# Performance work log

Hardware: AMD Instinct MI355X
Metric: run time of the kernel (lower is better)

The kernel has to match this reference:

```python
import jax, jax.numpy as jnp
import numpy as np
from math import sqrt

B, N, CS, H, D, K = 8, 256, 512, 8, 64, 32
NB = 2 * K + 1          # no_bins = 65
CT = 2048               # c_transition
INF = 1e9
WL = sqrt(0.5)          # w_L
EPS = 1e-5


def setup_inputs() -> dict:
    key = jax.random.key(0)
    ks = jax.random.split(key, 10)
    sc = 0.02
    return {
        "s": jax.random.normal(ks[0], (B, N, CS), jnp.float32),
        "masks": jnp.ones((B, N), jnp.bool_),
        "wq": jax.random.normal(ks[1], (CS, D * H), jnp.float32) * sc,
        "wk": jax.random.normal(ks[2], (CS, D * H), jnp.float32) * sc,
        "wv": jax.random.normal(ks[3], (CS, D * H), jnp.float32) * sc,
        "wb": jax.random.normal(ks[4], (NB, H), jnp.float32) * sc,
        "wo": jax.random.normal(ks[5], ((NB + D) * H, CS), jnp.float32) * sc,
        "bo": jnp.zeros((CS,), jnp.float32),
        "ln1_g": jnp.ones((CS,), jnp.float32),
        "ln1_b": jnp.zeros((CS,), jnp.float32),
        "w1": jax.random.normal(ks[6], (CS, CT), jnp.float32) * sc,
        "b1": jnp.zeros((CT,), jnp.float32),
        "w2": jax.random.normal(ks[7], (CT, CS), jnp.float32) * sc,
        "b2": jnp.zeros((CS,), jnp.float32),
        "ln2_g": jnp.ones((CS,), jnp.float32),
        "ln2_b": jnp.zeros((CS,), jnp.float32),
    }


def _layernorm(x, g, b):
    m = jnp.mean(x, -1, keepdims=True)
    v = jnp.var(x, -1, keepdims=True)
    return (x - m) * jax.lax.rsqrt(v + EPS) * g + b


def _heads(x):  # [B,N,D*H] -> [B,H,N,D]  (torch: reshape(B,N,D,H) then move H forward)
    return jnp.transpose(x.reshape(B, N, D, H), (0, 3, 1, 2))


def reference(s, masks, wq, wk, wv, wb, wo, bo, ln1_g, ln1_b, w1, b1, w2, b2, ln2_g, ln2_b):
    mf = masks.astype(s.dtype)                       # [B,N]
    sq = mf[:, :, None] * mf[:, None, :]             # [B,N,N]

    # relative position one-hot, clipped to [-K, K] -> [N,N,NB]
    r = jnp.arange(N)
    dmat = jnp.clip(r[:, None] - r[None, :], -K, K) + K
    relpos_base = jax.nn.one_hot(dmat, NB, dtype=s.dtype)
    relpos = relpos_base[None] * sq[..., None]       # [B,N,N,NB]

    b_bias = jnp.einsum('bijc,ch->bhij', relpos, wb)  # [B,H,N,N]

    q = _heads(s @ wq)                               # [B,H,N,D]
    k = _heads(s @ wk)
    v = _heads(s @ wv)

    logits = WL * (jnp.einsum('bhid,bhjd->bhij', q, k) / sqrt(D) + b_bias)
    logits = logits - INF * (1.0 - sq)[:, None]      # mask
    a = jax.nn.softmax(logits, axis=-1)              # [B,H,N,N]

    # pairwise aggregation and value aggregation (einsum avoids [B,H,N,N,NB] blowup)
    o_pair = jnp.einsum('bhij,bijc->bhic', a, relpos)  # [B,H,N,NB]
    o = jnp.einsum('bhij,bhjd->bhid', a, v)            # [B,H,N,D]

    op = jnp.transpose(o_pair, (0, 2, 1, 3)).reshape(B, N, H * NB)
    ov = jnp.transpose(o, (0, 2, 1, 3)).reshape(B, N, H * D)
    embd = jnp.concatenate([op, ov], axis=-1) @ wo + bo   # [B,N,CS]

    x = _layernorm(s + embd, ln1_g, ln1_b)
    ff = jax.nn.relu(x @ w1 + b1) @ w2 + b2
    x = _layernorm(x + ff, ln2_g, ln2_b)
    return x, a
```

## Files before the change

kernel.cpp:

```cpp
#include <hip/hip_runtime.h>
#include <hip/hip_bf16.h>
#include <cstdint>

#define B_ 8
#define N_ 256
#define CS_ 512
#define H_ 8
#define D_ 64
#define K_ 32
#define NB_ 65
#define CT_ 2048
#define WL_ 0.70710678118654752f

typedef __attribute__((ext_vector_type(8))) short bf16x8;
typedef __attribute__((ext_vector_type(4))) float f32x4;

#define GLOBAL_AS __attribute__((address_space(1)))
#define LDS_AS __attribute__((address_space(3)))

__device__ __forceinline__ void async16(void* lds, const void* g) {
  __builtin_amdgcn_global_load_lds((const GLOBAL_AS uint32_t*)g,
                                   (LDS_AS uint32_t*)lds, 16, 0, 0);
}

__device__ __forceinline__ ushort f2bf(float v) {
  __hip_bfloat16 hb = __float2bfloat16(v);
  return *(ushort*)&hb;
}

__device__ __forceinline__ float bf2f(ushort u) {
  union { uint32_t ui; float f; } cv; cv.ui = (uint32_t)u << 16;
  return cv.f;
}

__global__ __launch_bounds__(128) void gemm_bf16(
    const ushort* __restrict__ A, const ushort* __restrict__ Bt,
    const float* __restrict__ bias, float* __restrict__ C,
    ushort* __restrict__ Cb, int M, int Nc, int Kd, int flags) {
  __shared__ ushort As[2][64 * 64];
  __shared__ ushort Bs[2][128 * 64];
  int tid = threadIdx.x;
  int bm = blockIdx.y * 64, bn = blockIdx.x * 128;
  int S = gridDim.z, z = blockIdx.z;
  int T = Kd >> 6;
  int it0 = (z * T) / S, it1 = ((z + 1) * T) / S;
  if (flags & 8)  C  += (size_t)z * M * Nc;
  if (flags & 32) Cb += (size_t)z * M * Nc;
  int w = tid >> 6, l = tid & 63;
  int lm = l & 15, lq = l >> 4;
  int srow = tid >> 3;
  int sg = tid & 7;

  f32x4 acc[4][4];
#pragma unroll
  for (int i = 0; i < 4; ++i)
#pragma unroll
    for (int j = 0; j < 4; ++j) acc[i][j] = (f32x4){0.f, 0.f, 0.f, 0.f};

  {
    int k0 = it0 << 6;
#pragma unroll
    for (int r = 0; r < 4; ++r) {
      int row = r * 16 + srow;
      int gl = sg ^ (row & 7);
      async16(&As[0][row * 64 + sg * 8],
              A + (size_t)(bm + row) * Kd + k0 + gl * 8);
    }
#pragma unroll
    for (int r = 0; r < 8; ++r) {
      int row = r * 16 + srow;
      int gl = sg ^ (row & 7);
      async16(&Bs[0][row * 64 + sg * 8],
              Bt + (size_t)(bn + row) * Kd + k0 + gl * 8);
    }
  }
  for (int it = it0; it < it1; ++it) {
    int cur = (it - it0) & 1;
    __syncthreads();
    if (it + 1 < it1) {
      int nxt = cur ^ 1;
      int k0 = (it + 1) << 6;
#pragma unroll
      for (int r = 0; r < 4; ++r) {
        int row = r * 16 + srow;
        int gl = sg ^ (row & 7);
        async16(&As[nxt][row * 64 + sg * 8],
                A + (size_t)(bm + row) * Kd + k0 + gl * 8);
      }
#pragma unroll
      for (int r = 0; r < 8; ++r) {
        int row = r * 16 + srow;
        int gl = sg ^ (row & 7);
        async16(&Bs[nxt][row * 64 + sg * 8],
                Bt + (size_t)(bn + row) * Kd + k0 + gl * 8);
      }
    }
#pragma unroll
    for (int kk = 0; kk < 2; ++kk) {
      bf16x8 af[4], bfr[4];
#pragma unroll
      for (int i = 0; i < 4; ++i) {
        int ma = 16 * i + lm;
        af[i] = *(const bf16x8*)&As[cur][ma * 64 + ((kk * 4 + lq) ^ (ma & 7)) * 8];
        int nb = w * 64 + 16 * i + lm;
        bfr[i] = *(const bf16x8*)&Bs[cur][nb * 64 + ((kk * 4 + lq) ^ (nb & 7)) * 8];
      }
#pragma unroll
      for (int i = 0; i < 4; ++i)
#pragma unroll
        for (int j = 0; j < 4; ++j)
          acc[i][j] = __builtin_amdgcn_mfma_f32_16x16x32_bf16(
              af[i], bfr[j], acc[i][j], 0, 0, 0);
    }
  }
  __syncthreads();

  int bcol0 = bn + w * 64;
  int lr = l >> 3, lc = l & 7;
  ushort* Tb = &Bs[0][w * 4096];

  if (flags & 16) {
    int which = bcol0 >> 9;
    int hh = (bcol0 & 511) >> 6;
    int b = bm >> 8, nn0 = bm & 255;
    if (which == 2) {
#pragma unroll
      for (int j = 0; j < 4; ++j)
#pragma unroll
        for (int i = 0; i < 4; ++i) {
          ushort pk[4];
#pragma unroll
          for (int r = 0; r < 4; ++r) pk[r] = f2bf(acc[i][j][r]);
          *(uint2*)&Tb[(16 * j + lm) * 64 + 16 * i + lq * 4] = *(uint2*)pk;
        }
    } else {
#pragma unroll
      for (int j = 0; j < 4; ++j)
#pragma unroll
        for (int i = 0; i < 4; ++i)
#pragma unroll
          for (int r = 0; r < 4; ++r)
            Tb[(16 * i + lq * 4 + r) * 64 + 16 * j + lm] = f2bf(acc[i][j][r]);
    }
    __asm__ __volatile__("" ::: "memory");
    ushort* dstb = Cb + (size_t)which * 1048576 + (size_t)(b * 8 + hh) * 16384;
#pragma unroll
    for (int p = 0; p < 8; ++p) {
      int rowL = p * 8 + lr;
      bf16x8 vv = *(const bf16x8*)&Tb[rowL * 64 + lc * 8];
      if (which == 2)
        *(bf16x8*)(dstb + (size_t)rowL * 256 + nn0 + lc * 8) = vv;
      else
        *(bf16x8*)(dstb + (size_t)(nn0 + rowL) * 64 + lc * 8) = vv;
    }
    return;
  }
  if (flags & 4) {
#pragma unroll
    for (int j = 0; j < 4; ++j) {
      float bv = ((flags & 1) && z == 0) ? bias[bcol0 + 16 * j + lm] : 0.f;
#pragma unroll
      for (int i = 0; i < 4; ++i)
#pragma unroll
        for (int r = 0; r < 4; ++r) {
          float v = acc[i][j][r] + bv;
          if (flags & 2) v = fmaxf(v, 0.f);
          Tb[(16 * i + lq * 4 + r) * 64 + 16 * j + lm] = f2bf(v);
        }
    }
    __asm__ __volatile__("" ::: "memory");
#pragma unroll
    for (int p = 0; p < 8; ++p) {
      int rowL = p * 8 + lr;
      bf16x8 vv = *(const bf16x8*)&Tb[rowL * 64 + lc * 8];
      *(bf16x8*)(Cb + (size_t)(bm + rowL) * Nc + bcol0 + lc * 8) = vv;
    }
    return;
  }
#pragma unroll
  for (int j = 0; j < 4; ++j) {
    int col = bcol0 + 16 * j + lm;
    float bv = ((flags & 1) && z == 0) ? bias[col] : 0.f;
#pragma unroll
    for (int i = 0; i < 4; ++i)
#pragma unroll
      for (int r = 0; r < 4; ++r) {
        int row = bm + 16 * i + lq * 4 + r;
        float v = acc[i][j][r] + bv;
        if (flags & 2) v = fmaxf(v, 0.f);
        C[(size_t)row * Nc + col] = v;
      }
  }
}

__global__ __launch_bounds__(256) void prep_all(
    const float* __restrict__ s, __hip_bfloat16* __restrict__ s_bf,
    const float* __restrict__ wq, const float* __restrict__ wk,
    const float* __restrict__ wv, const float* __restrict__ wo,
    const float* __restrict__ w1, const float* __restrict__ w2,
    __hip_bfloat16* __restrict__ wqkvT, __hip_bfloat16* __restrict__ wopT,
    __hip_bfloat16* __restrict__ w1T, __hip_bfloat16* __restrict__ w2T) {
  int blk = blockIdx.x;
  if (blk < 512) {
    int i = blk * 256 + threadIdx.x;
    float4 a = ((const float4*)s)[i * 2];
    float4 c = ((const float4*)s)[i * 2 + 1];
    ushort pk[8] = {f2bf(a.x), f2bf(a.y), f2bf(a.z), f2bf(a.w),
                    f2bf(c.x), f2bf(c.y), f2bf(c.z), f2bf(c.w)};
    *(uint4*)&((ushort*)s_bf)[i * 8] = *(uint4*)pk;
    return;
  }
  blk -= 512;
  __shared__ float tile[32][33];
  const float* src;
  __hip_bfloat16* dst;
  int R, C, Kpad, tX, tIdx, whichBase = -1;
  if (blk < 768) {
    int zz = blk >> 8; tIdx = blk & 255;
    src = zz == 0 ? wq : zz == 1 ? wk : wv;
    dst = wqkvT; whichBase = zz * 512; R = 512; C = 512; Kpad = 512; tX = 16;
  } else if (blk < 1312) {
    tIdx = blk - 768; src = wo; dst = wopT; R = 1032; C = 512; Kpad = 1088; tX = 16;
  } else if (blk < 2336) {
    tIdx = blk - 1312; src = w1; dst = w1T; R = 512; C = 2048; Kpad = 512; tX = 64;
  } else {
    tIdx = blk - 2336; src = w2; dst = w2T; R = 2048; C = 512; Kpad = 2048; tX = 16;
  }
  int c0 = (tIdx % tX) * 32, r0 = (tIdx / tX) * 32;
  int tx = threadIdx.x & 31, ty = threadIdx.x >> 5;
#pragma unroll
  for (int yy = 0; yy < 32; yy += 8) {
    int r = r0 + ty + yy, c = c0 + tx;
    tile[ty + yy][tx] = (r < R && c < C) ? src[(size_t)r * C + c] : 0.f;
  }
  __syncthreads();
#pragma unroll
  for (int yy = 0; yy < 32; yy += 8) {
    int cc = c0 + ty + yy, k = r0 + tx;
    if (cc < C && k < Kpad) {
      int n = (whichBase >= 0) ? (whichBase + (cc & 7) * 64 + (cc >> 3)) : cc;
      dst[(size_t)n * Kpad + k] = __float2bfloat16(tile[tx][ty + yy]);
    }
  }
}

__global__ __launch_bounds__(128) void attn_fused(
    const ushort* __restrict__ qh, const ushort* __restrict__ kh,
    const ushort* __restrict__ vT, const int* __restrict__ masks,
    const float* __restrict__ wb, float* __restrict__ a_out,
    ushort* __restrict__ cat) {
  int strip = blockIdx.x & 7, bh = blockIdx.x >> 3;
  int h = bh & 7, b = bh >> 3;
  __shared__ ushort Ks[256 * 64];
  __shared__ ushort Ps[32 * 64];
  __shared__ float wbs[NB_];
  __shared__ float mfj[256];
  int tid = threadIdx.x;
  int srow = tid >> 3, sg = tid & 7;
#pragma unroll
  for (int rr = 0; rr < 16; ++rr) {
    int row = rr * 16 + srow;
    int gl = sg ^ (row & 7);
    async16(&Ks[row * 64 + sg * 8],
            kh + ((size_t)bh * 256 + row) * 64 + gl * 8);
  }
  int w = tid >> 6, l = tid & 63, lm = l & 15, lq = l >> 4;
  bf16x8 qf[2];
  {
    const ushort* qrow =
        qh + ((size_t)bh * 256 + strip * 32 + w * 16 + lm) * 64 + lq * 8;
    qf[0] = *(const bf16x8*)qrow;
    qf[1] = *(const bf16x8*)(qrow + 32);
  }
  if (tid < NB_) wbs[tid] = wb[tid * H_ + h];
  mfj[tid]       = (masks[b * 256 + tid] != 0) ? 1.f : 0.f;
  mfj[tid + 128] = (masks[b * 256 + tid + 128] != 0) ? 1.f : 0.f;
  __syncthreads();

  f32x4 acc[16];
#pragma unroll
  for (int ct = 0; ct < 16; ++ct) {
    int krow = ct * 16 + lm;
    bf16x8 kf0 = *(const bf16x8*)&Ks[krow * 64 + ((lq) ^ (krow & 7)) * 8];
    bf16x8 kf1 = *(const bf16x8*)&Ks[krow * 64 + ((4 + lq) ^ (krow & 7)) * 8];
    f32x4 zf = (f32x4){0.f, 0.f, 0.f, 0.f};
    zf = __builtin_amdgcn_mfma_f32_16x16x32_bf16(qf[0], kf0, zf, 0, 0, 0);
    acc[ct] = __builtin_amdgcn_mfma_f32_16x16x32_bf16(qf[1], kf1, zf, 0, 0, 0);
  }
  int ibase = strip * 32 + w * 16 + lq * 4;
  float mfi[4];
#pragma unroll
  for (int r = 0; r < 4; ++r) mfi[r] = mfj[ibase + r];
#pragma unroll
  for (int ct = 0; ct < 16; ++ct) {
    int j = ct * 16 + lm;
    float mj = mfj[j];
#pragma unroll
    for (int r = 0; r < 4; ++r) {
      int i = ibase + r;
      int diff = i - j;
      int cb = diff < -K_ ? 0 : (diff > K_ ? 2 * K_ : diff + K_);
      float sq = mfi[r] * mj;
      acc[ct][r] = WL_ * (acc[ct][r] * 0.125f + wbs[cb] * sq) - 1e9f * (1.f - sq);
    }
  }
  float mx[4], sm[4];
#pragma unroll
  for (int r = 0; r < 4; ++r) {
    float m = acc[0][r];
#pragma unroll
    for (int ct = 1; ct < 16; ++ct) m = fmaxf(m, acc[ct][r]);
#pragma unroll
    for (int o = 1; o < 16; o <<= 1) m = fmaxf(m, __shfl_xor(m, o, 64));
    mx[r] = m;
  }
#pragma unroll
  for (int ct = 0; ct < 16; ++ct)
#pragma unroll
    for (int r = 0; r < 4; ++r) acc[ct][r] = __expf(acc[ct][r] - mx[r]);
#pragma unroll
  for (int r = 0; r < 4; ++r) {
    float s = 0.f;
#pragma unroll
    for (int ct = 0; ct < 16; ++ct) s += acc[ct][r];
#pragma unroll
    for (int o = 1; o < 16; o <<= 1) s += __shfl_xor(s, o, 64);
    sm[r] = 1.f / s;
  }
  float p0[4] = {0.f, 0.f, 0.f, 0.f}, p64[4] = {0.f, 0.f, 0.f, 0.f};
#pragma unroll
  for (int ct = 0; ct < 16; ++ct) {
    int j = ct * 16 + lm;
    float mj = mfj[j];
#pragma unroll
    for (int r = 0; r < 4; ++r) {
      int i = ibase + r;
      float aval = acc[ct][r] * sm[r];
      a_out[((size_t)bh * 256 + i) * 256 + j] = aval;
      float val = aval * mfi[r] * mj;
      int diff = i - j;
      if (diff <= -K_)      p0[r] += val;
      else if (diff >= K_)  p64[r] += val;
      else cat[((size_t)(b * 256 + i)) * 1088 + h * 65 + diff + K_] = f2bf(val);
    }
  }
#pragma unroll
  for (int r = 0; r < 4; ++r)
#pragma unroll
    for (int o = 1; o < 16; o <<= 1) {
      p0[r]  += __shfl_xor(p0[r], o, 64);
      p64[r] += __shfl_xor(p64[r], o, 64);
    }
  if (lm == 0) {
#pragma unroll
    for (int r = 0; r < 4; ++r) {
      int i = ibase + r;
      cat[((size_t)(b * 256 + i)) * 1088 + h * 65 + 0]      = f2bf(p0[r]);
      cat[((size_t)(b * 256 + i)) * 1088 + h * 65 + 2 * K_] = f2bf(p64[r]);
    }
  }
#pragma unroll
  for (int r = 0; r < 4; ++r) {
    int i = ibase + r;
#pragma unroll
    for (int t = 0; t < 4; ++t) {
      int c = 1 + lm + 16 * t;
      if (c < 64) {
        int j = i - c + K_;
        if (j < 0 || j > 255)
          cat[((size_t)(b * 256 + i)) * 1088 + h * 65 + c] = 0;
      }
    }
  }
  if (h == 0) {
    for (int idx = tid; idx < 32 * 56; idx += 128) {
      int r = idx / 56, c = 1032 + (idx - r * 56);
      cat[((size_t)(b * 256 + strip * 32 + r)) * 1088 + c] = 0;
    }
  }
  f32x4 acc2[4];
#pragma unroll
  for (int nt = 0; nt < 4; ++nt) acc2[nt] = (f32x4){0.f, 0.f, 0.f, 0.f};
  const ushort* vbase = vT + (size_t)bh * 16384;
#pragma unroll
  for (int qt = 0; qt < 4; ++qt) {
    bf16x8 vf0[4], vf1[4];
#pragma unroll
    for (int nt = 0; nt < 4; ++nt) {
      const ushort* vrow = vbase + (size_t)(nt * 16 + lm) * 256 + qt * 64 + lq * 8;
      vf0[nt] = *(const bf16x8*)vrow;
      vf1[nt] = *(const bf16x8*)(vrow + 32);
    }
#pragma unroll
    for (int ctl = 0; ctl < 4; ++ctl) {
      int ct = qt * 4 + ctl;
#pragma unroll
      for (int r = 0; r < 4; ++r) {
        int rowl = w * 16 + lq * 4 + r;
        int g = ctl * 2 + (lm >> 3);
        Ps[rowl * 64 + ((g ^ (rowl & 7)) << 3) + (lm & 7)] =
            f2bf(acc[ct][r] * sm[r]);
      }
    }
    int prow = w * 16 + lm;
#pragma unroll
    for (int kst = 0; kst < 2; ++kst) {
      bf16x8 af = *(const bf16x8*)&Ps[prow * 64 + (((kst * 4 + lq) ^ (prow & 7)) << 3)];
#pragma unroll
      for (int nt = 0; nt < 4; ++nt)
        acc2[nt] = __builtin_amdgcn_mfma_f32_16x16x32_bf16(
            af, kst ? vf1[nt] : vf0[nt], acc2[nt], 0, 0, 0);
    }
  }
#pragma unroll
  for (int nt = 0; nt < 4; ++nt) {
    int d = nt * 16 + lm;
#pragma unroll
    for (int r = 0; r < 4; ++r) {
      int i = ibase + r;
      cat[((size_t)(b * 256 + i)) * 1088 + 520 + h * 64 + d] = f2bf(acc2[nt][r]);
    }
  }
}

__global__ __launch_bounds__(128) void ln_sum(
    const float* __restrict__ x1, const ushort* __restrict__ xp,
    int S, int stride, const float* __restrict__ g,
    const float* __restrict__ bta, float* __restrict__ out,
    __hip_bfloat16* __restrict__ out_bf) {
  __shared__ float redA[2], redB[2];
  int row = blockIdx.x, tid = threadIdx.x;
  size_t base = (size_t)row * 512;
  float4 v = *(const float4*)(x1 + base + tid * 4);
  for (int s = 0; s < S; ++s) {
    uint2 p = *(const uint2*)(xp + (size_t)s * stride + base + tid * 4);
    v.x += bf2f((ushort)(p.x & 0xffff));
    v.y += bf2f((ushort)(p.x >> 16));
    v.z += bf2f((ushort)(p.y & 0xffff));
    v.w += bf2f((ushort)(p.y >> 16));
  }
  float su = v.x + v.y + v.z + v.w;
  float sq = v.x * v.x + v.y * v.y + v.z * v.z + v.w * v.w;
#pragma unroll
  for (int o = 32; o > 0; o >>= 1) {
    su += __shfl_xor(su, o, 64);
    sq += __shfl_xor(sq, o, 64);
  }
  int w = tid >> 6;
  if ((tid & 63) == 0) { redA[w] = su; redB[w] = sq; }
  __syncthreads();
  su = redA[0] + redA[1]; sq = redB[0] + redB[1];
  float mean = su * (1.f / 512.f);
  float var = sq * (1.f / 512.f) - mean * mean;
  float inv = rsqrtf(var + 1e-5f);
  float4 gv = *(const float4*)(g + tid * 4);
  float4 bv = *(const float4*)(bta + tid * 4);
  float4 o4;
  o4.x = (v.x - mean) * inv * gv.x + bv.x;
  o4.y = (v.y - mean) * inv * gv.y + bv.y;
  o4.z = (v.z - mean) * inv * gv.z + bv.z;
  o4.w = (v.w - mean) * inv * gv.w + bv.w;
  *(float4*)(out + base + tid * 4) = o4;
  if (out_bf) {
    ushort pk[4] = {f2bf(o4.x), f2bf(o4.y), f2bf(o4.z), f2bf(o4.w)};
    *(uint2*)&((ushort*)out_bf)[base + tid * 4] = *(uint2*)pk;
  }
}

extern "C" void kernel_launch(void* const* d_in, const int* in_sizes, int n_in,
                              void* d_out, int out_size, void* d_ws, size_t ws_size,
                              hipStream_t stream) {
  const float* s     = (const float*)d_in[0];
  const int*   masks = (const int*)d_in[1];
  const float* wq = (const float*)d_in[2];
  const float* wk = (const float*)d_in[3];
  const float* wv = (const float*)d_in[4];
  const float* wb = (const float*)d_in[5];
  const float* wo = (const float*)d_in[6];
  const float* bo = (const float*)d_in[7];
  const float* ln1_g = (const float*)d_in[8];
  const float* ln1_b = (const float*)d_in[9];
  const float* w1 = (const float*)d_in[10];
  const float* b1 = (const float*)d_in[11];
  const float* w2 = (const float*)d_in[12];
  const float* b2 = (const float*)d_in[13];
  const float* ln2_g = (const float*)d_in[14];
  const float* ln2_b = (const float*)d_in[15];

  float* out_x = (float*)d_out;
  float* out_a = out_x + 1048576;

  float* ws = (float*)d_ws;
  ushort* embd_part = (ushort*)(ws + 0);
  float* xbuf       = ws + 4194304;
  ushort* ff_part   = (ushort*)(ws + 5242880);
  ushort* qkv_bf    = (ushort*)(ws + 9437184);
  ushort* q_bf = qkv_bf;
  ushort* k_bf = qkv_bf + 1048576;
  ushort* v_bf = qkv_bf + 2097152;
  ushort* cat_bf = (ushort*)(ws + 10223616);
  __hip_bfloat16* h_bf  = (__hip_bfloat16*)(ws + 11337728);
  __hip_bfloat16* s_bf  = (__hip_bfloat16*)(ws + 13434880);
  __hip_bfloat16* x_bf  = (__hip_bfloat16*)(ws + 13959168);
  __hip_bfloat16* wqkvT = (__hip_bfloat16*)(ws + 14483456);
  __hip_bfloat16* wopT  = (__hip_bfloat16*)(ws + 14876672);
  __hip_bfloat16* w1T   = (__hip_bfloat16*)(ws + 15155200);
  __hip_bfloat16* w2T   = (__hip_bfloat16*)(ws + 15679488);

  dim3 blk(256), blkg(128);
  prep_all<<<dim3(3872), blk, 0, stream>>>(s, s_bf, wq, wk, wv, wo, w1, w2,
                                           wqkvT, wopT, w1T, w2T);
  gemm_bf16<<<dim3(12, 32, 1), blkg, 0, stream>>>(
      (const ushort*)s_bf, (const ushort*)wqkvT, nullptr, nullptr,
      qkv_bf, 2048, 1536, 512, 16);
  attn_fused<<<dim3(512), blkg, 0, stream>>>(q_bf, k_bf, v_bf, masks, wb,
                                             out_a, cat_bf);
  gemm_bf16<<<dim3(4, 32, 4), blkg, 0, stream>>>(
      cat_bf, (const ushort*)wopT, bo, nullptr, embd_part,
      2048, 512, 1088, 1 | 4 | 32);
  ln_sum<<<dim3(2048), blkg, 0, stream>>>(s, embd_part, 4, 1048576,
                                          ln1_g, ln1_b, xbuf, x_bf);
  gemm_bf16<<<dim3(16, 32, 1), blkg, 0, stream>>>(
      (const ushort*)x_bf, (const ushort*)w1T, b1, nullptr, (ushort*)h_bf,
      2048, 2048, 512, 1 | 2 | 4);
  gemm_bf16<<<dim3(4, 32, 4), blkg, 0, stream>>>(
      (const ushort*)h_bf, (const ushort*)w2T, b2, nullptr, ff_part,
      2048, 512, 2048, 1 | 4 | 32);
  ln_sum<<<dim3(2048), blkg, 0, stream>>>(xbuf, ff_part, 4, 1048576,
                                          ln2_g, ln2_b, out_x, nullptr);
}
```

Measured before the change: 178.6 us.

## Fuse all stages into one persistent kernel with software grid barriers

```diff
diff --git a/kernel.cpp b/kernel.cpp
--- a/kernel.cpp
+++ b/kernel.cpp
@@ -11,6 +11,7 @@
 #define NB_ 65
 #define CT_ 2048
 #define WL_ 0.70710678118654752f
+#define NBLK 512
 
 typedef __attribute__((ext_vector_type(8))) short bf16x8;
 typedef __attribute__((ext_vector_type(4))) float f32x4;
@@ -33,18 +34,38 @@
   return cv.f;
 }
 
-__global__ __launch_bounds__(128) void gemm_bf16(
+__device__ unsigned g_cnt = 0, g_gen = 0;
+
+__device__ __forceinline__ void gridbar(int tid) {
+  __syncthreads();
+  if (tid == 0) {
+    unsigned g = __hip_atomic_load(&g_gen, __ATOMIC_RELAXED,
+                                   __HIP_MEMORY_SCOPE_AGENT);
+    unsigned v = __hip_atomic_fetch_add(&g_cnt, 1u, __ATOMIC_ACQ_REL,
+                                        __HIP_MEMORY_SCOPE_AGENT);
+    if (v == NBLK - 1u) {
+      __hip_atomic_store(&g_cnt, 0u, __ATOMIC_RELAXED,
+                         __HIP_MEMORY_SCOPE_AGENT);
+      __hip_atomic_store(&g_gen, g + 1u, __ATOMIC_RELEASE,
+                         __HIP_MEMORY_SCOPE_AGENT);
+    } else {
+      while (__hip_atomic_load(&g_gen, __ATOMIC_RELAXED,
+                               __HIP_MEMORY_SCOPE_AGENT) == g)
+        __builtin_amdgcn_s_sleep(8);
+      __builtin_amdgcn_fence(__ATOMIC_ACQUIRE, "agent");
+    }
+  }
+  __syncthreads();
+}
+
+__device__ __forceinline__ void gemm_stage(
     const ushort* __restrict__ A, const ushort* __restrict__ Bt,
-    const float* __restrict__ bias, float* __restrict__ C,
-    ushort* __restrict__ Cb, int M, int Nc, int Kd, int flags) {
-  __shared__ ushort As[2][64 * 64];
-  __shared__ ushort Bs[2][128 * 64];
-  int tid = threadIdx.x;
-  int bm = blockIdx.y * 64, bn = blockIdx.x * 128;
-  int S = gridDim.z, z = blockIdx.z;
+    const float* __restrict__ bias, ushort* __restrict__ Cb,
+    int M, int Nc, int Kd, int flags, int bx, int by, int z, int S,
+    ushort* As, ushort* Bs, int tid) {
+  int bm = by * 64, bn = bx * 128;
   int T = Kd >> 6;
   int it0 = (z * T) / S, it1 = ((z + 1) * T) / S;
-  if (flags & 8)  C  += (size_t)z * M * Nc;
   if (flags & 32) Cb += (size_t)z * M * Nc;
   int w = tid >> 6, l = tid & 63;
   int lm = l & 15, lq = l >> 4;
@@ -63,14 +84,14 @@
     for (int r = 0; r < 4; ++r) {
       int row = r * 16 + srow;
       int gl = sg ^ (row & 7);
-      async16(&As[0][row * 64 + sg * 8],
+      async16(&As[row * 64 + sg * 8],
               A + (size_t)(bm + row) * Kd + k0 + gl * 8);
     }
 #pragma unroll
     for (int r = 0; r < 8; ++r) {
       int row = r * 16 + srow;
       int gl = sg ^ (row & 7);
-      async16(&Bs[0][row * 64 + sg * 8],
+      async16(&Bs[row * 64 + sg * 8],
               Bt + (size_t)(bn + row) * Kd + k0 + gl * 8);
     }
   }
@@ -84,14 +105,14 @@
       for (int r = 0; r < 4; ++r) {
         int row = r * 16 + srow;
         int gl = sg ^ (row & 7);
-        async16(&As[nxt][row * 64 + sg * 8],
+        async16(&As[nxt * 4096 + row * 64 + sg * 8],
                 A + (size_t)(bm + row) * Kd + k0 + gl * 8);
       }
 #pragma unroll
       for (int r = 0; r < 8; ++r) {
         int row = r * 16 + srow;
         int gl = sg ^ (row & 7);
-        async16(&Bs[nxt][row * 64 + sg * 8],
+        async16(&Bs[nxt * 8192 + row * 64 + sg * 8],
                 Bt + (size_t)(bn + row) * Kd + k0 + gl * 8);
       }
     }
@@ -101,9 +122,11 @@
 #pragma unroll
       for (int i = 0; i < 4; ++i) {
         int ma = 16 * i + lm;
-        af[i] = *(const bf16x8*)&As[cur][ma * 64 + ((kk * 4 + lq) ^ (ma & 7)) * 8];
+        af[i] = *(const bf16x8*)&As[cur * 4096 + ma * 64 +
+                                    ((kk * 4 + lq) ^ (ma & 7)) * 8];
         int nb = w * 64 + 16 * i + lm;
-        bfr[i] = *(const bf16x8*)&Bs[cur][nb * 64 + ((kk * 4 + lq) ^ (nb & 7)) * 8];
+        bfr[i] = *(const bf16x8*)&Bs[cur * 8192 + nb * 64 +
+                                     ((kk * 4 + lq) ^ (nb & 7)) * 8];
       }
 #pragma unroll
       for (int i = 0; i < 4; ++i)
@@ -117,7 +140,7 @@
 
   int bcol0 = bn + w * 64;
   int lr = l >> 3, lc = l & 7;
-  ushort* Tb = &Bs[0][w * 4096];
+  ushort* Tb = Bs + w * 4096;
 
   if (flags & 16) {
     int which = bcol0 >> 9;
@@ -155,107 +178,35 @@
     }
     return;
   }
-  if (flags & 4) {
-#pragma unroll
-    for (int j = 0; j < 4; ++j) {
-      float bv = ((flags & 1) && z == 0) ? bias[bcol0 + 16 * j + lm] : 0.f;
-#pragma unroll
-      for (int i = 0; i < 4; ++i)
-#pragma unroll
-        for (int r = 0; r < 4; ++r) {
-          float v = acc[i][j][r] + bv;
-          if (flags & 2) v = fmaxf(v, 0.f);
-          Tb[(16 * i + lq * 4 + r) * 64 + 16 * j + lm] = f2bf(v);
-        }
-    }
-    __asm__ __volatile__("" ::: "memory");
-#pragma unroll
-    for (int p = 0; p < 8; ++p) {
-      int rowL = p * 8 + lr;
-      bf16x8 vv = *(const bf16x8*)&Tb[rowL * 64 + lc * 8];
-      *(bf16x8*)(Cb + (size_t)(bm + rowL) * Nc + bcol0 + lc * 8) = vv;
-    }
-    return;
-  }
 #pragma unroll
   for (int j = 0; j < 4; ++j) {
-    int col = bcol0 + 16 * j + lm;
-    float bv = ((flags & 1) && z == 0) ? bias[col] : 0.f;
+    float bv = ((flags & 1) && z == 0) ? bias[bcol0 + 16 * j + lm] : 0.f;
 #pragma unroll
     for (int i = 0; i < 4; ++i)
 #pragma unroll
       for (int r = 0; r < 4; ++r) {
-        int row = bm + 16 * i + lq * 4 + r;
         float v = acc[i][j][r] + bv;
         if (flags & 2) v = fmaxf(v, 0.f);
-        C[(size_t)row * Nc + col] = v;
-      }
-  }
-}
-
-__global__ __launch_bounds__(256) void prep_all(
-    const float* __restrict__ s, __hip_bfloat16* __restrict__ s_bf,
-    const float* __restrict__ wq, const float* __restrict__ wk,
-    const float* __restrict__ wv, const float* __restrict__ wo,
-    const float* __restrict__ w1, const float* __restrict__ w2,
-    __hip_bfloat16* __restrict__ wqkvT, __hip_bfloat16* __restrict__ wopT,
-    __hip_bfloat16* __restrict__ w1T, __hip_bfloat16* __restrict__ w2T) {
-  int blk = blockIdx.x;
-  if (blk < 512) {
-    int i = blk * 256 + threadIdx.x;
-    float4 a = ((const float4*)s)[i * 2];
-    float4 c = ((const float4*)s)[i * 2 + 1];
-    ushort pk[8] = {f2bf(a.x), f2bf(a.y), f2bf(a.z), f2bf(a.w),
-                    f2bf(c.x), f2bf(c.y), f2bf(c.z), f2bf(c.w)};
-    *(uint4*)&((ushort*)s_bf)[i * 8] = *(uint4*)pk;
-    return;
-  }
-  blk -= 512;
-  __shared__ float tile[32][33];
-  const float* src;
-  __hip_bfloat16* dst;
-  int R, C, Kpad, tX, tIdx, whichBase = -1;
-  if (blk < 768) {
-    int zz = blk >> 8; tIdx = blk & 255;
-    src = zz == 0 ? wq : zz == 1 ? wk : wv;
-    dst = wqkvT; whichBase = zz * 512; R = 512; C = 512; Kpad = 512; tX = 16;
-  } else if (blk < 1312) {
-    tIdx = blk - 768; src = wo; dst = wopT; R = 1032; C = 512; Kpad = 1088; tX = 16;
-  } else if (blk < 2336) {
-    tIdx = blk - 1312; src = w1; dst = w1T; R = 512; C = 2048; Kpad = 512; tX = 64;
-  } else {
-    tIdx = blk - 2336; src = w2; dst = w2T; R = 2048; C = 512; Kpad = 2048; tX = 16;
-  }
-  int c0 = (tIdx % tX) * 32, r0 = (tIdx / tX) * 32;
-  int tx = threadIdx.x & 31, ty = threadIdx.x >> 5;
-#pragma unroll
-  for (int yy = 0; yy < 32; yy += 8) {
-    int r = r0 + ty + yy, c = c0 + tx;
-    tile[ty + yy][tx] = (r < R && c < C) ? src[(size_t)r * C + c] : 0.f;
-  }
-  __syncthreads();
-#pragma unroll
-  for (int yy = 0; yy < 32; yy += 8) {
-    int cc = c0 + ty + yy, k = r0 + tx;
-    if (cc < C && k < Kpad) {
-      int n = (whichBase >= 0) ? (whichBase + (cc & 7) * 64 + (cc >> 3)) : cc;
-      dst[(size_t)n * Kpad + k] = __float2bfloat16(tile[tx][ty + yy]);
-    }
-  }
-}
-
-__global__ __launch_bounds__(128) void attn_fused(
+        Tb[(16 * i + lq * 4 + r) * 64 + 16 * j + lm] = f2bf(v);
+      }
+  }
+  __asm__ __volatile__("" ::: "memory");
+#pragma unroll
+  for (int p = 0; p < 8; ++p) {
+    int rowL = p * 8 + lr;
+    bf16x8 vv = *(const bf16x8*)&Tb[rowL * 64 + lc * 8];
+    *(bf16x8*)(Cb + (size_t)(bm + rowL) * Nc + bcol0 + lc * 8) = vv;
+  }
+}
+
+__device__ __forceinline__ void attn_stage(
     const ushort* __restrict__ qh, const ushort* __restrict__ kh,
     const ushort* __restrict__ vT, const int* __restrict__ masks,
     const float* __restrict__ wb, float* __restrict__ a_out,
-    ushort* __restrict__ cat) {
-  int strip = blockIdx.x & 7, bh = blockIdx.x >> 3;
+    ushort* __restrict__ cat, ushort* Ks, ushort* Ps, float* wbs, float* mfj,
+    int blk, int tid) {
+  int strip = blk & 7, bh = blk >> 3;
   int h = bh & 7, b = bh >> 3;
-  __shared__ ushort Ks[256 * 64];
-  __shared__ ushort Ps[32 * 64];
-  __shared__ float wbs[NB_];
-  __shared__ float mfj[256];
-  int tid = threadIdx.x;
   int srow = tid >> 3, sg = tid & 7;
 #pragma unroll
   for (int rr = 0; rr < 16; ++rr) {
@@ -423,13 +374,11 @@
   }
 }
 
-__global__ __launch_bounds__(128) void ln_sum(
+__device__ __forceinline__ void ln_stage(
     const float* __restrict__ x1, const ushort* __restrict__ xp,
     int S, int stride, const float* __restrict__ g,
     const float* __restrict__ bta, float* __restrict__ out,
-    __hip_bfloat16* __restrict__ out_bf) {
-  __shared__ float redA[2], redB[2];
-  int row = blockIdx.x, tid = threadIdx.x;
+    __hip_bfloat16* __restrict__ out_bf, int row, float* red, int tid) {
   size_t base = (size_t)row * 512;
   float4 v = *(const float4*)(x1 + base + tid * 4);
   for (int s = 0; s < S; ++s) {
@@ -447,9 +396,9 @@
     sq += __shfl_xor(sq, o, 64);
   }
   int w = tid >> 6;
-  if ((tid & 63) == 0) { redA[w] = su; redB[w] = sq; }
+  if ((tid & 63) == 0) { red[w] = su; red[2 + w] = sq; }
   __syncthreads();
-  su = redA[0] + redA[1]; sq = redB[0] + redB[1];
+  su = red[0] + red[1]; sq = red[2] + red[3];
   float mean = su * (1.f / 512.f);
   float var = sq * (1.f / 512.f) - mean * mean;
   float inv = rsqrtf(var + 1e-5f);
@@ -465,11 +414,140 @@
     ushort pk[4] = {f2bf(o4.x), f2bf(o4.y), f2bf(o4.z), f2bf(o4.w)};
     *(uint2*)&((ushort*)out_bf)[base + tid * 4] = *(uint2*)pk;
   }
+  __syncthreads();
+}
+
+__global__ __launch_bounds__(128, 1) void fused_all(
+    const float* __restrict__ s, const int* __restrict__ masks,
+    const float* __restrict__ wq, const float* __restrict__ wk,
+    const float* __restrict__ wv, const float* __restrict__ wb,
+    const float* __restrict__ wo, const float* __restrict__ bo,
+    const float* __restrict__ ln1_g, const float* __restrict__ ln1_b,
+    const float* __restrict__ w1, const float* __restrict__ b1,
+    const float* __restrict__ w2, const float* __restrict__ b2,
+    const float* __restrict__ ln2_g, const float* __restrict__ ln2_b,
+    float* __restrict__ out_x, float* __restrict__ out_a,
+    float* __restrict__ ws) {
+  __shared__ __align__(16) uint8_t Lraw[57344];
+  ushort* As  = (ushort*)Lraw;
+  ushort* Bs  = (ushort*)(Lraw + 16384);
+  ushort* Ks  = (ushort*)Lraw;
+  ushort* Ps  = (ushort*)(Lraw + 32768);
+  float*  wbs = (float*)(Lraw + 36864);
+  float*  mfj = (float*)(Lraw + 37376);
+  float*  red = (float*)(Lraw + 38400);
+  float (*tile)[33] = (float(*)[33])Lraw;
+
+  int blk = blockIdx.x, tid = threadIdx.x;
+
+  ushort* embd_part = (ushort*)(ws + 0);
+  float* xbuf       = ws + 4194304;
+  ushort* ff_part   = (ushort*)(ws + 5242880);
+  ushort* qkv_bf    = (ushort*)(ws + 9437184);
+  ushort* q_bf = qkv_bf;
+  ushort* k_bf = qkv_bf + 1048576;
+  ushort* v_bf = qkv_bf + 2097152;
+  ushort* cat_bf = (ushort*)(ws + 10223616);
+  ushort* h_bf   = (ushort*)(ws + 11337728);
+  ushort* s_bf   = (ushort*)(ws + 13434880);
+  ushort* x_bf   = (ushort*)(ws + 13959168);
+  ushort* wqkvT  = (ushort*)(ws + 14483456);
+  ushort* wopT   = (ushort*)(ws + 14876672);
+  ushort* w1T    = (ushort*)(ws + 15155200);
+  ushort* w2T    = (ushort*)(ws + 15679488);
+
+  {
+    int i0 = blk * 256 + tid;
+#pragma unroll
+    for (int p = 0; p < 2; ++p) {
+      int i = i0 + p * 128;
+      float4 a = ((const float4*)s)[(size_t)i * 2];
+      float4 c = ((const float4*)s)[(size_t)i * 2 + 1];
+      ushort pk[8] = {f2bf(a.x), f2bf(a.y), f2bf(a.z), f2bf(a.w),
+                      f2bf(c.x), f2bf(c.y), f2bf(c.z), f2bf(c.w)};
+      *(uint4*)&s_bf[(size_t)i * 8] = *(uint4*)pk;
+    }
+    for (int t = blk; t < 3360; t += NBLK) {
+      const float* src; ushort* dst;
+      int R, C, Kpad, tX, tIdx, whichBase = -1;
+      if (t < 768) {
+        int zz = t >> 8; tIdx = t & 255;
+        src = zz == 0 ? wq : zz == 1 ? wk : wv;
+        dst = wqkvT; whichBase = zz * 512; R = 512; C = 512; Kpad = 512; tX = 16;
+      } else if (t < 1312) {
+        tIdx = t - 768; src = wo; dst = wopT; R = 1032; C = 512; Kpad = 1088; tX = 16;
+      } else if (t < 2336) {
+        tIdx = t - 1312; src = w1; dst = w1T; R = 512; C = 2048; Kpad = 512; tX = 64;
+      } else {
+        tIdx = t - 2336; src = w2; dst = w2T; R = 2048; C = 512; Kpad = 2048; tX = 16;
+      }
+      int c0 = (tIdx % tX) * 32, r0 = (tIdx / tX) * 32;
+      int tx = tid & 7, ty = tid >> 3;
+      __syncthreads();
+#pragma unroll
+      for (int yy = 0; yy < 32; yy += 16) {
+        int r = r0 + yy + ty, c = c0 + tx * 4;
+        float4 v = (r < R) ? *(const float4*)&src[(size_t)r * C + c]
+                           : (float4){0.f, 0.f, 0.f, 0.f};
+        tile[yy + ty][tx * 4 + 0] = v.x;
+        tile[yy + ty][tx * 4 + 1] = v.y;
+        tile[yy + ty][tx * 4 + 2] = v.z;
+        tile[yy + ty][tx * 4 + 3] = v.w;
+      }
+      __syncthreads();
+#pragma unroll
+      for (int yy = 0; yy < 32; yy += 16) {
+        int cc = c0 + yy + ty;
+        int k = r0 + tx * 4;
+        float a0 = tile[tx * 4 + 0][yy + ty];
+        float a1 = tile[tx * 4 + 1][yy + ty];
+        float a2 = tile[tx * 4 + 2][yy + ty];
+        float a3 = tile[tx * 4 + 3][yy + ty];
+        int n = (whichBase >= 0) ? (whichBase + (cc & 7) * 64 + (cc >> 3)) : cc;
+        ushort pk[4] = {f2bf(a0), f2bf(a1), f2bf(a2), f2bf(a3)};
+        *(uint2*)&dst[(size_t)n * Kpad + k] = *(uint2*)pk;
+      }
+    }
+  }
+  gridbar(tid);
+
+  if (blk < 384)
+    gemm_stage(s_bf, wqkvT, nullptr, qkv_bf, 2048, 1536, 512, 16,
+               blk % 12, blk / 12, 0, 1, As, Bs, tid);
+  gridbar(tid);
+
+  attn_stage(q_bf, k_bf, v_bf, masks, wb, out_a, cat_bf,
+             Ks, Ps, wbs, mfj, blk, tid);
+  gridbar(tid);
+
+  gemm_stage(cat_bf, wopT, bo, embd_part, 2048, 512, 1088, 1 | 4 | 32,
+             blk & 3, (blk >> 2) & 31, blk >> 7, 4, As, Bs, tid);
+  gridbar(tid);
+
+#pragma unroll
+  for (int rr = 0; rr < 4; ++rr)
+    ln_stage(s, embd_part, 4, 1048576, ln1_g, ln1_b, xbuf,
+             (__hip_bfloat16*)x_bf, blk + rr * NBLK, red, tid);
+  gridbar(tid);
+
+  gemm_stage(x_bf, w1T, b1, h_bf, 2048, 2048, 512, 1 | 2 | 4,
+             blk & 15, blk >> 4, 0, 1, As, Bs, tid);
+  gridbar(tid);
+
+  gemm_stage(h_bf, w2T, b2, ff_part, 2048, 512, 2048, 1 | 4 | 32,
+             blk & 3, (blk >> 2) & 31, blk >> 7, 4, As, Bs, tid);
+  gridbar(tid);
+
+#pragma unroll
+  for (int rr = 0; rr < 4; ++rr)
+    ln_stage(xbuf, ff_part, 4, 1048576, ln2_g, ln2_b, out_x,
+             nullptr, blk + rr * NBLK, red, tid);
 }
 
 extern "C" void kernel_launch(void* const* d_in, const int* in_sizes, int n_in,
                               void* d_out, int out_size, void* d_ws, size_t ws_size,
                               hipStream_t stream) {
+  (void)in_sizes; (void)n_in; (void)out_size; (void)ws_size;
   const float* s     = (const float*)d_in[0];
   const int*   masks = (const int*)d_in[1];
   const float* wq = (const float*)d_in[2];
@@ -490,42 +568,7 @@
   float* out_x = (float*)d_out;
   float* out_a = out_x + 1048576;
 
-  float* ws = (float*)d_ws;
-  ushort* embd_part = (ushort*)(ws + 0);
-  float* xbuf       = ws + 4194304;
-  ushort* ff_part   = (ushort*)(ws + 5242880);
-  ushort* qkv_bf    = (ushort*)(ws + 9437184);
-  ushort* q_bf = qkv_bf;
-  ushort* k_bf = qkv_bf + 1048576;
-  ushort* v_bf = qkv_bf + 2097152;
-  ushort* cat_bf = (ushort*)(ws + 10223616);
-  __hip_bfloat16* h_bf  = (__hip_bfloat16*)(ws + 11337728);
-  __hip_bfloat16* s_bf  = (__hip_bfloat16*)(ws + 13434880);
-  __hip_bfloat16* x_bf  = (__hip_bfloat16*)(ws + 13959168);
-  __hip_bfloat16* wqkvT = (__hip_bfloat16*)(ws + 14483456);
-  __hip_bfloat16* wopT  = (__hip_bfloat16*)(ws + 14876672);
-  __hip_bfloat16* w1T   = (__hip_bfloat16*)(ws + 15155200);
-  __hip_bfloat16* w2T   = (__hip_bfloat16*)(ws + 15679488);
-
-  dim3 blk(256), blkg(128);
-  prep_all<<<dim3(3872), blk, 0, stream>>>(s, s_bf, wq, wk, wv, wo, w1, w2,
-                                           wqkvT, wopT, w1T, w2T);
-  gemm_bf16<<<dim3(12, 32, 1), blkg, 0, stream>>>(
-      (const ushort*)s_bf, (const ushort*)wqkvT, nullptr, nullptr,
-      qkv_bf, 2048, 1536, 512, 16);
-  attn_fused<<<dim3(512), blkg, 0, stream>>>(q_bf, k_bf, v_bf, masks, wb,
-                                             out_a, cat_bf);
-  gemm_bf16<<<dim3(4, 32, 4), blkg, 0, stream>>>(
-      cat_bf, (const ushort*)wopT, bo, nullptr, embd_part,
-      2048, 512, 1088, 1 | 4 | 32);
-  ln_sum<<<dim3(2048), blkg, 0, stream>>>(s, embd_part, 4, 1048576,
-                                          ln1_g, ln1_b, xbuf, x_bf);
-  gemm_bf16<<<dim3(16, 32, 1), blkg, 0, stream>>>(
-      (const ushort*)x_bf, (const ushort*)w1T, b1, nullptr, (ushort*)h_bf,
-      2048, 2048, 512, 1 | 2 | 4);
-  gemm_bf16<<<dim3(4, 32, 4), blkg, 0, stream>>>(
-      (const ushort*)h_bf, (const ushort*)w2T, b2, nullptr, ff_part,
-      2048, 512, 2048, 1 | 4 | 32);
-  ln_sum<<<dim3(2048), blkg, 0, stream>>>(xbuf, ff_part, 4, 1048576,
-                                          ln2_g, ln2_b, out_x, nullptr);
-}
+  fused_all<<<dim3(NBLK), dim3(128), 0, stream>>>(
+      s, masks, wq, wk, wv, wb, wo, bo, ln1_g, ln1_b, w1, b1, w2, b2,
+      ln2_g, ln2_b, out_x, out_a, (float*)d_ws);
+}
```

Result: slower. 518.6 us (+190.3%).
